# Kernel tuning notes

Hardware: AMD Instinct MI355X
Metric: run time of the kernel (lower is better)

## Reference

```python
import jax, jax.numpy as jnp
import numpy as np

HEADS = 16  # init_kwargs['heads']


def setup_inputs() -> dict:
    key = jax.random.key(0)
    k1, k2, k3, k4, k5, k6 = jax.random.split(key, 6)
    N, L, E = 2, 2048, 1024
    return {
        "values": jax.random.normal(k1, (N, L, E), dtype=jnp.float32),
        "key": jax.random.normal(k2, (N, L, E), dtype=jnp.float32),
        "query": jax.random.normal(k3, (N, L, E), dtype=jnp.float32),
        "mask": jax.random.randint(k4, (N, 1, L, L), 0, 2, dtype=jnp.int32),
        # fc_out: Linear(heads*head_dim=E, E) with bias
        "W_out": jax.random.normal(k5, (E, E), dtype=jnp.float32) / np.sqrt(E),
        "b_out": jax.random.normal(k6, (E,), dtype=jnp.float32) * 0.01,
    }


def reference(values, key, query, mask, W_out, b_out):
    N, Lq, E = query.shape
    Lk = key.shape[1]
    H = HEADS
    D = E // H  # head_dim = 64
    q = query.reshape(N, Lq, H, D)
    k = key.reshape(N, Lk, H, D)
    v = values.reshape(N, Lk, H, D)
    # energy: (N, H, Q, K)
    energy = jnp.einsum("nqhd,nkhd->nhqk", q, k)
    # masked_fill BEFORE scaling, as in the original
    energy = jnp.where(mask == 0, jnp.float32(-1e20), energy)
    attn = jax.nn.softmax(energy / np.float32(np.sqrt(D)), axis=3)
    out = jnp.einsum("nhqk,nkhd->nqhd", attn, v).reshape(N, Lq, H * D)
    return out @ W_out.T + b_out
```

## Files before the change

### kernel.cpp

```cpp
#include <hip/hip_runtime.h>

#define L_SEQ  2048
#define EMB    1024
#define NHEAD  16
#define HDIM   64
#define NBATCH 2

typedef unsigned short u16;
typedef unsigned int   u32;
typedef unsigned long long u64;
typedef short bf16x8 __attribute__((ext_vector_type(8)));
typedef float f32x4  __attribute__((ext_vector_type(4)));
typedef int   i32x4  __attribute__((ext_vector_type(4)));

static __device__ __forceinline__ u16 f2bf(float x) {
    union { float f; unsigned u; } a; a.f = x;
    unsigned r = a.u + 0x7FFFu + ((a.u >> 16) & 1u);
    return (u16)(r >> 16);
}
static __device__ __forceinline__ void cvt8(const float4& a, const float4& b, u16* o, float s) {
    o[0]=f2bf(a.x*s); o[1]=f2bf(a.y*s); o[2]=f2bf(a.z*s); o[3]=f2bf(a.w*s);
    o[4]=f2bf(b.x*s); o[5]=f2bf(b.y*s); o[6]=f2bf(b.z*s); o[7]=f2bf(b.w*s);
}

static __device__ __forceinline__ u32 cvt_pk_bf16(float lo, float hi) {
    u32 r;
    asm("v_cvt_pk_bf16_f32 %0, %1, %2" : "=v"(r) : "v"(lo), "v"(hi));
    return r;
}
static __device__ __forceinline__ void permswap32(u32 &x, u32 &y) {
    asm("v_permlane32_swap_b32 %0, %1" : "+v"(x), "+v"(y));
}
static __device__ __forceinline__ void permswap16(u32 &x, u32 &y) {
    asm("v_permlane16_swap_b32 %0, %1" : "+v"(x), "+v"(y));
}

__global__ void pack_mask(const int* __restrict__ Mg, u64* __restrict__ maskp)
{
    const int wave = threadIdx.x >> 6;
    const int lane = threadIdx.x & 63;
    const int row  = blockIdx.x * 4 + wave;
    const int* mp = Mg + (size_t)row * L_SEQ + lane;
    u64* op = maskp + (size_t)row * (L_SEQ / 64);
    for (int t = 0; t < L_SEQ / 64; ++t) {
        u64 b = __ballot(mp[t * 64] != 0);
        if (lane == 0) op[t] = b;
    }
}

__global__ __launch_bounds__(256)
void prep_qkv(const float* __restrict__ Qg, const float* __restrict__ Kg,
              const float* __restrict__ Vg, u16* __restrict__ Qb,
              u16* __restrict__ Kb, u16* __restrict__ Vt)
{
    const int t = blockIdx.x, h = blockIdx.y, n = blockIdx.z;
    const int tid = threadIdx.x;
    const int row = tid >> 2;
    const int dc  = (tid & 3) * 16;

    __shared__ u16 Vl2[64][72];

    const size_t gin = ((size_t)(n * L_SEQ) + t * 64 + row) * EMB + h * HDIM + dc;

    {
        const float qs = 0.125f * 1.44269504f;
        u16 o[16];
        cvt8(*(const float4*)(Qg + gin),     *(const float4*)(Qg + gin + 4),  o,     qs);
        cvt8(*(const float4*)(Qg + gin + 8), *(const float4*)(Qg + gin + 12), o + 8, qs);
        *(uint4*)(Qb + gin)     = *(const uint4*)o;
        *(uint4*)(Qb + gin + 8) = *(const uint4*)&o[8];
    }
    {
        u16 o[16];
        cvt8(*(const float4*)(Kg + gin),     *(const float4*)(Kg + gin + 4),  o,     1.f);
        cvt8(*(const float4*)(Kg + gin + 8), *(const float4*)(Kg + gin + 12), o + 8, 1.f);
        size_t ko = ((size_t)(n * NHEAD + h) * L_SEQ + t * 64 + row) * HDIM + dc;
        *(uint4*)(Kb + ko)     = *(const uint4*)o;
        *(uint4*)(Kb + ko + 8) = *(const uint4*)&o[8];
    }
    {
        u16 o[16];
        cvt8(*(const float4*)(Vg + gin),     *(const float4*)(Vg + gin + 4),  o,     1.f);
        cvt8(*(const float4*)(Vg + gin + 8), *(const float4*)(Vg + gin + 12), o + 8, 1.f);
        #pragma unroll
        for (int j = 0; j < 16; ++j) Vl2[dc + j][row] = o[j];
    }
    __syncthreads();
    {
        const int d  = tid >> 2;
        const int kc = (tid & 3) * 16;
        size_t vo = ((size_t)(n * NHEAD + h) * HDIM + d) * L_SEQ + t * 64 + kc;
        *(uint4*)(Vt + vo)     = *(const uint4*)&Vl2[d][kc];
        *(uint4*)(Vt + vo + 8) = *(const uint4*)&Vl2[d][kc + 8];
    }
}

__global__ void wcvt(const float* __restrict__ W, u16* __restrict__ Wb)
{
    int i = (blockIdx.x * 256 + threadIdx.x) * 8;
    float4 a = *(const float4*)(W + i);
    float4 b = *(const float4*)(W + i + 4);
    u16 o[8];
    cvt8(a, b, o, 1.f);
    *(uint4*)(Wb + i) = *(const uint4*)o;
}

__global__ __launch_bounds__(256, 4)
void attn_kernel(const u16* __restrict__ Qb, const u16* __restrict__ Kb,
                 const u16* __restrict__ Vt, const u64* __restrict__ maskp,
                 u16* __restrict__ Og)
{
    const int qblk = blockIdx.x;
    const int h    = blockIdx.y;
    const int n    = blockIdx.z;
    const int tid  = threadIdx.x;
    const int wave = tid >> 6;
    const int lane = tid & 63;
    const int l16  = lane & 15;
    const int quad = lane >> 4;

    __shared__ u16 Kl[64][72];
    __shared__ u16 Vl[64][72];

    const int q0 = qblk * 64 + wave * 16;

    bf16x8 qf[2];
    {
        const u16* qp = Qb + ((size_t)(n * L_SEQ) + q0 + l16) * EMB + h * HDIM;
        qf[0] = *(const bf16x8*)(qp + quad * 8);
        qf[1] = *(const bf16x8*)(qp + 32 + quad * 8);
    }

    f32x4 acc[4];
    #pragma unroll
    for (int c = 0; c < 4; ++c)
        #pragma unroll
        for (int r = 0; r < 4; ++r) acc[c][r] = 0.f;
    float lsum = 0.f;

    const u16* kbase = Kb + (size_t)(n * NHEAD + h) * L_SEQ * HDIM;
    const u16* vbase = Vt + (size_t)(n * NHEAD + h) * HDIM * L_SEQ;
    const u64* mbase = maskp + ((size_t)(n * L_SEQ) + q0 + l16) * (L_SEQ / 64);

    const int srow = tid >> 2;
    const int scol = (tid & 3) * 16;

    uint4 kr0, kr1, vr0, vr1;
    u64 mr;

    {
        const u16* kp = kbase + (size_t)srow * HDIM + scol;
        const u16* vp = vbase + (size_t)srow * L_SEQ + scol;
        kr0 = *(const uint4*)kp;  kr1 = *(const uint4*)(kp + 8);
        vr0 = *(const uint4*)vp;  vr1 = *(const uint4*)(vp + 8);
        mr  = mbase[0];
    }

    for (int t = 0; t < L_SEQ / 64; ++t) {
        __syncthreads();
        *(uint4*)&Kl[srow][scol]     = kr0;
        *(uint4*)&Kl[srow][scol + 8] = kr1;
        *(uint4*)&Vl[srow][scol]     = vr0;
        *(uint4*)&Vl[srow][scol + 8] = vr1;
        u64 mcur = mr;

        if (t + 1 < L_SEQ / 64) {
            const u16* kp = kbase + (size_t)((t + 1) * 64 + srow) * HDIM + scol;
            const u16* vp = vbase + (size_t)srow * L_SEQ + (t + 1) * 64 + scol;
            kr0 = *(const uint4*)kp;  kr1 = *(const uint4*)(kp + 8);
            vr0 = *(const uint4*)vp;  vr1 = *(const uint4*)(vp + 8);
            mr  = mbase[t + 1];
        }
        __syncthreads();

        f32x4 St[4];
        #pragma unroll
        for (int cc = 0; cc < 4; ++cc) {
            bf16x8 k0 = *(const bf16x8*)&Kl[cc * 16 + l16][quad * 8];
            bf16x8 k1 = *(const bf16x8*)&Kl[cc * 16 + l16][32 + quad * 8];
            f32x4 z; z[0]=0.f; z[1]=0.f; z[2]=0.f; z[3]=0.f;
            z = __builtin_amdgcn_mfma_f32_16x16x32_bf16(k0, qf[0], z, 0, 0, 0);
            z = __builtin_amdgcn_mfma_f32_16x16x32_bf16(k1, qf[1], z, 0, 0, 0);
            St[cc] = z;
        }

        u32 lo  = (u32)(mcur >> (quad * 4));
        u32 hiw = (u32)(mcur >> (quad * 4 + 32));
        u32 Dw[8];
        #pragma unroll
        for (int cc = 0; cc < 4; ++cc) {
            u32 w = (cc < 2) ? lo : hiw;
            float pv[4];
            #pragma unroll
            for (int r = 0; r < 4; ++r) {
                const int pos = (cc & 1) * 16 + r;
                int sm = (int)(w << (31 - pos)) >> 31;
                float p = __builtin_amdgcn_exp2f(St[cc][r]);
                p = __int_as_float(__float_as_int(p) & sm);
                lsum += p;
                pv[r] = p;
            }
            Dw[2 * cc]     = cvt_pk_bf16(pv[0], pv[1]);
            Dw[2 * cc + 1] = cvt_pk_bf16(pv[2], pv[3]);
        }

        #pragma unroll
        for (int kc = 0; kc < 2; ++kc) {
            u32 b0 = Dw[4 * kc + 0], b2 = Dw[4 * kc + 2];
            permswap32(b0, b2); permswap16(b0, b2);
            u32 b1 = Dw[4 * kc + 1], b3 = Dw[4 * kc + 3];
            permswap32(b1, b3); permswap16(b1, b3);
            union { i32x4 i; bf16x8 v; } pu;
            pu.i[0] = (int)b0; pu.i[1] = (int)b1; pu.i[2] = (int)b2; pu.i[3] = (int)b3;
            bf16x8 pf = pu.v;
            #pragma unroll
            for (int dc = 0; dc < 4; ++dc) {
                bf16x8 vf = *(const bf16x8*)&Vl[dc * 16 + l16][kc * 32 + quad * 8];
                acc[dc] = __builtin_amdgcn_mfma_f32_16x16x32_bf16(vf, pf, acc[dc], 0, 0, 0);
            }
        }
    }

    float s = lsum;
    s += __shfl_xor(s, 16);
    s += __shfl_xor(s, 32);
    float inv = 1.f / s;

    u16* op = Og + ((size_t)(n * L_SEQ) + q0 + l16) * EMB + h * HDIM + quad * 4;
    #pragma unroll
    for (int dc = 0; dc < 4; ++dc) {
        u32 u0 = cvt_pk_bf16(acc[dc][0] * inv, acc[dc][1] * inv);
        u32 u1 = cvt_pk_bf16(acc[dc][2] * inv, acc[dc][3] * inv);
        uint2 st; st.x = u0; st.y = u1;
        *(uint2*)(op + dc * 16) = st;
    }
}

__global__ __launch_bounds__(256, 4)
void out_gemm(const u16* __restrict__ A, const u16* __restrict__ B,
              const float* __restrict__ bias, float* __restrict__ out)
{
    const int bn  = blockIdx.x;
    const int bm  = blockIdx.y;
    const int tid = threadIdx.x;
    const int wave = tid >> 6;
    const int lane = tid & 63;
    const int l16  = lane & 15;
    const int quad = lane >> 4;
    const int wr = wave >> 1, wc = wave & 1;

    __shared__ u16 Al[64][72];
    __shared__ u16 Bl[64][72];

    f32x4 acc[2][2];
    #pragma unroll
    for (int i = 0; i < 2; ++i)
        #pragma unroll
        for (int j = 0; j < 2; ++j)
            #pragma unroll
            for (int r = 0; r < 4; ++r) acc[i][j][r] = 0.f;

    const int srow = tid >> 2;
    const int kc   = (tid & 3) * 16;

    const u16* ap = A + (size_t)(bm * 64 + srow) * EMB + kc;
    const u16* bp = B + (size_t)(bn * 64 + srow) * EMB + kc;

    uint4 ar0 = *(const uint4*)ap,        ar1 = *(const uint4*)(ap + 8);
    uint4 br0 = *(const uint4*)bp,        br1 = *(const uint4*)(bp + 8);

    for (int k0 = 0; k0 < EMB; k0 += 64) {
        __syncthreads();
        *(uint4*)&Al[srow][kc]     = ar0;
        *(uint4*)&Al[srow][kc + 8] = ar1;
        *(uint4*)&Bl[srow][kc]     = br0;
        *(uint4*)&Bl[srow][kc + 8] = br1;
        if (k0 + 64 < EMB) {
            ar0 = *(const uint4*)(ap + k0 + 64);  ar1 = *(const uint4*)(ap + k0 + 72);
            br0 = *(const uint4*)(bp + k0 + 64);  br1 = *(const uint4*)(bp + k0 + 72);
        }
        __syncthreads();

        #pragma unroll
        for (int kk = 0; kk < 2; ++kk) {
            bf16x8 af[2], bfr[2];
            #pragma unroll
            for (int i = 0; i < 2; ++i)
                af[i] = *(const bf16x8*)&Al[wr * 32 + i * 16 + l16][kk * 32 + quad * 8];
            #pragma unroll
            for (int j = 0; j < 2; ++j)
                bfr[j] = *(const bf16x8*)&Bl[wc * 32 + j * 16 + l16][kk * 32 + quad * 8];
            #pragma unroll
            for (int i = 0; i < 2; ++i)
                #pragma unroll
                for (int j = 0; j < 2; ++j)
                    acc[i][j] = __builtin_amdgcn_mfma_f32_16x16x32_bf16(af[i], bfr[j], acc[i][j], 0, 0, 0);
        }
    }

    #pragma unroll
    for (int j = 0; j < 2; ++j) {
        int col = bn * 64 + wc * 32 + j * 16 + l16;
        float bv = bias[col];
        #pragma unroll
        for (int i = 0; i < 2; ++i) {
            int row0 = bm * 64 + wr * 32 + i * 16 + quad * 4;
            #pragma unroll
            for (int r = 0; r < 4; ++r)
                out[(size_t)(row0 + r) * EMB + col] = acc[i][j][r] + bv;
        }
    }
}

extern "C" void kernel_launch(void* const* d_in, const int* in_sizes, int n_in,
                              void* d_out, int out_size, void* d_ws, size_t ws_size,
                              hipStream_t stream)
{
    const float* Vg = (const float*)d_in[0];
    const float* Kg = (const float*)d_in[1];
    const float* Qg = (const float*)d_in[2];
    const int*   Mg = (const int*)d_in[3];
    const float* Wg = (const float*)d_in[4];
    const float* Bg = (const float*)d_in[5];
    float* Og = (float*)d_out;

    const size_t QKV = (size_t)NBATCH * L_SEQ * EMB;
    char* ws = (char*)d_ws;
    u16* attn_ws = (u16*)ws;
    u16* Wb      = (u16*)(ws + QKV * 2);
    u16* Qb      = (u16*)(ws + QKV * 2 + 2 * 1024 * 1024);
    u16* Kb      = Qb + QKV;
    u16* Vt      = Kb + QKV;
    u64* maskp   = (u64*)(Vt + QKV);

    pack_mask<<<dim3(NBATCH * L_SEQ / 4), 256, 0, stream>>>(Mg, maskp);
    prep_qkv<<<dim3(L_SEQ / 64, NHEAD, NBATCH), 256, 0, stream>>>(Qg, Kg, Vg, Qb, Kb, Vt);
    wcvt<<<dim3(EMB * EMB / (256 * 8)), 256, 0, stream>>>(Wg, Wb);

    dim3 g1(L_SEQ / 64, NHEAD, NBATCH);
    attn_kernel<<<g1, 256, 0, stream>>>(Qb, Kb, Vt, maskp, attn_ws);

    dim3 g2(EMB / 64, (NBATCH * L_SEQ) / 64);
    out_gemm<<<g2, 256, 0, stream>>>(attn_ws, Wb, Bg, Og);
}
```

Before: 220.5 us.

## Process two query sub-tiles per wave to reuse K/V tiles across 128 queries

Each attention block now handles 128 queries instead of 64, and each wave computes two 16-row query sub-tiles against the same K and V fragments read from shared memory. This halves the global K/V loads and LDS traffic per query and doubles the MFMA work per LDS read. In exchange, register use per thread grows (two accumulator sets), so the launch bound drops to 2 blocks per CU, and the grid halves to 512 blocks, which reduces parallelism and the ability to hide latency.

```diff
diff --git a/kernel.cpp b/kernel.cpp
--- a/kernel.cpp
+++ b/kernel.cpp
@@ -105,7 +105,7 @@
     *(uint4*)(Wb + i) = *(const uint4*)o;
 }
 
-__global__ __launch_bounds__(256, 4)
+__global__ __launch_bounds__(256, 2)
 void attn_kernel(const u16* __restrict__ Qb, const u16* __restrict__ Kb,
                  const u16* __restrict__ Vt, const u64* __restrict__ maskp,
                  u16* __restrict__ Og)
@@ -122,38 +122,43 @@
     __shared__ u16 Kl[64][72];
     __shared__ u16 Vl[64][72];
 
-    const int q0 = qblk * 64 + wave * 16;
-
-    bf16x8 qf[2];
-    {
-        const u16* qp = Qb + ((size_t)(n * L_SEQ) + q0 + l16) * EMB + h * HDIM;
-        qf[0] = *(const bf16x8*)(qp + quad * 8);
-        qf[1] = *(const bf16x8*)(qp + 32 + quad * 8);
-    }
-
-    f32x4 acc[4];
-    #pragma unroll
-    for (int c = 0; c < 4; ++c)
-        #pragma unroll
-        for (int r = 0; r < 4; ++r) acc[c][r] = 0.f;
-    float lsum = 0.f;
+    const int q0 = qblk * 128 + wave * 32;
+
+    bf16x8 qf[2][2];
+    #pragma unroll
+    for (int qs = 0; qs < 2; ++qs) {
+        const u16* qp = Qb + ((size_t)(n * L_SEQ) + q0 + qs * 16 + l16) * EMB + h * HDIM;
+        qf[qs][0] = *(const bf16x8*)(qp + quad * 8);
+        qf[qs][1] = *(const bf16x8*)(qp + 32 + quad * 8);
+    }
+
+    f32x4 acc[2][4];
+    #pragma unroll
+    for (int qs = 0; qs < 2; ++qs)
+        #pragma unroll
+        for (int c = 0; c < 4; ++c)
+            #pragma unroll
+            for (int r = 0; r < 4; ++r) acc[qs][c][r] = 0.f;
+    float lsum[2] = {0.f, 0.f};
 
     const u16* kbase = Kb + (size_t)(n * NHEAD + h) * L_SEQ * HDIM;
     const u16* vbase = Vt + (size_t)(n * NHEAD + h) * HDIM * L_SEQ;
     const u64* mbase = maskp + ((size_t)(n * L_SEQ) + q0 + l16) * (L_SEQ / 64);
+    const int  mqs   = 16 * (L_SEQ / 64);
 
     const int srow = tid >> 2;
     const int scol = (tid & 3) * 16;
 
     uint4 kr0, kr1, vr0, vr1;
-    u64 mr;
+    u64 mr[2];
 
     {
         const u16* kp = kbase + (size_t)srow * HDIM + scol;
         const u16* vp = vbase + (size_t)srow * L_SEQ + scol;
         kr0 = *(const uint4*)kp;  kr1 = *(const uint4*)(kp + 8);
         vr0 = *(const uint4*)vp;  vr1 = *(const uint4*)(vp + 8);
-        mr  = mbase[0];
+        mr[0] = mbase[0];
+        mr[1] = mbase[mqs];
     }
 
     for (int t = 0; t < L_SEQ / 64; ++t) {
@@ -162,77 +167,91 @@
         *(uint4*)&Kl[srow][scol + 8] = kr1;
         *(uint4*)&Vl[srow][scol]     = vr0;
         *(uint4*)&Vl[srow][scol + 8] = vr1;
-        u64 mcur = mr;
+        u64 mcur0 = mr[0], mcur1 = mr[1];
 
         if (t + 1 < L_SEQ / 64) {
             const u16* kp = kbase + (size_t)((t + 1) * 64 + srow) * HDIM + scol;
             const u16* vp = vbase + (size_t)srow * L_SEQ + (t + 1) * 64 + scol;
             kr0 = *(const uint4*)kp;  kr1 = *(const uint4*)(kp + 8);
             vr0 = *(const uint4*)vp;  vr1 = *(const uint4*)(vp + 8);
-            mr  = mbase[t + 1];
+            mr[0] = mbase[t + 1];
+            mr[1] = mbase[mqs + t + 1];
         }
         __syncthreads();
 
-        f32x4 St[4];
+        const int sh = quad * 4;
+        u32 mlo[2], mhi[2];
+        mlo[0] = (u32)mcur0 >> sh;  mhi[0] = (u32)(mcur0 >> 32) >> sh;
+        mlo[1] = (u32)mcur1 >> sh;  mhi[1] = (u32)(mcur1 >> 32) >> sh;
+
+        u32 Dw[2][8];
         #pragma unroll
         for (int cc = 0; cc < 4; ++cc) {
             bf16x8 k0 = *(const bf16x8*)&Kl[cc * 16 + l16][quad * 8];
             bf16x8 k1 = *(const bf16x8*)&Kl[cc * 16 + l16][32 + quad * 8];
-            f32x4 z; z[0]=0.f; z[1]=0.f; z[2]=0.f; z[3]=0.f;
-            z = __builtin_amdgcn_mfma_f32_16x16x32_bf16(k0, qf[0], z, 0, 0, 0);
-            z = __builtin_amdgcn_mfma_f32_16x16x32_bf16(k1, qf[1], z, 0, 0, 0);
-            St[cc] = z;
-        }
-
-        u32 lo  = (u32)(mcur >> (quad * 4));
-        u32 hiw = (u32)(mcur >> (quad * 4 + 32));
-        u32 Dw[8];
-        #pragma unroll
-        for (int cc = 0; cc < 4; ++cc) {
-            u32 w = (cc < 2) ? lo : hiw;
-            float pv[4];
-            #pragma unroll
-            for (int r = 0; r < 4; ++r) {
-                const int pos = (cc & 1) * 16 + r;
-                int sm = (int)(w << (31 - pos)) >> 31;
-                float p = __builtin_amdgcn_exp2f(St[cc][r]);
-                p = __int_as_float(__float_as_int(p) & sm);
-                lsum += p;
-                pv[r] = p;
+            f32x4 z0; z0[0]=0.f; z0[1]=0.f; z0[2]=0.f; z0[3]=0.f;
+            f32x4 z1 = z0;
+            z0 = __builtin_amdgcn_mfma_f32_16x16x32_bf16(k0, qf[0][0], z0, 0, 0, 0);
+            z0 = __builtin_amdgcn_mfma_f32_16x16x32_bf16(k1, qf[0][1], z0, 0, 0, 0);
+            z1 = __builtin_amdgcn_mfma_f32_16x16x32_bf16(k0, qf[1][0], z1, 0, 0, 0);
+            z1 = __builtin_amdgcn_mfma_f32_16x16x32_bf16(k1, qf[1][1], z1, 0, 0, 0);
+
+            #pragma unroll
+            for (int qs = 0; qs < 2; ++qs) {
+                const f32x4& z = (qs == 0) ? z0 : z1;
+                u32 w = (cc < 2) ? mlo[qs] : mhi[qs];
+                float pv[4];
+                #pragma unroll
+                for (int r = 0; r < 4; ++r) {
+                    const int pos = (cc & 1) * 16 + r;
+                    int sm = (int)(w << (31 - pos)) >> 31;
+                    float p = __builtin_amdgcn_exp2f(z[r]);
+                    p = __int_as_float(__float_as_int(p) & sm);
+                    lsum[qs] += p;
+                    pv[r] = p;
+                }
+                Dw[qs][2 * cc]     = cvt_pk_bf16(pv[0], pv[1]);
+                Dw[qs][2 * cc + 1] = cvt_pk_bf16(pv[2], pv[3]);
             }
-            Dw[2 * cc]     = cvt_pk_bf16(pv[0], pv[1]);
-            Dw[2 * cc + 1] = cvt_pk_bf16(pv[2], pv[3]);
         }
 
         #pragma unroll
         for (int kc = 0; kc < 2; ++kc) {
-            u32 b0 = Dw[4 * kc + 0], b2 = Dw[4 * kc + 2];
-            permswap32(b0, b2); permswap16(b0, b2);
-            u32 b1 = Dw[4 * kc + 1], b3 = Dw[4 * kc + 3];
-            permswap32(b1, b3); permswap16(b1, b3);
-            union { i32x4 i; bf16x8 v; } pu;
-            pu.i[0] = (int)b0; pu.i[1] = (int)b1; pu.i[2] = (int)b2; pu.i[3] = (int)b3;
-            bf16x8 pf = pu.v;
+            bf16x8 pf[2];
+            #pragma unroll
+            for (int qs = 0; qs < 2; ++qs) {
+                u32 b0 = Dw[qs][4 * kc + 0], b2 = Dw[qs][4 * kc + 2];
+                permswap32(b0, b2); permswap16(b0, b2);
+                u32 b1 = Dw[qs][4 * kc + 1], b3 = Dw[qs][4 * kc + 3];
+                permswap32(b1, b3); permswap16(b1, b3);
+                union { i32x4 i; bf16x8 v; } pu;
+                pu.i[0] = (int)b0; pu.i[1] = (int)b1; pu.i[2] = (int)b2; pu.i[3] = (int)b3;
+                pf[qs] = pu.v;
+            }
             #pragma unroll
             for (int dc = 0; dc < 4; ++dc) {
                 bf16x8 vf = *(const bf16x8*)&Vl[dc * 16 + l16][kc * 32 + quad * 8];
-                acc[dc] = __builtin_amdgcn_mfma_f32_16x16x32_bf16(vf, pf, acc[dc], 0, 0, 0);
+                acc[0][dc] = __builtin_amdgcn_mfma_f32_16x16x32_bf16(vf, pf[0], acc[0][dc], 0, 0, 0);
+                acc[1][dc] = __builtin_amdgcn_mfma_f32_16x16x32_bf16(vf, pf[1], acc[1][dc], 0, 0, 0);
             }
         }
     }
 
-    float s = lsum;
-    s += __shfl_xor(s, 16);
-    s += __shfl_xor(s, 32);
-    float inv = 1.f / s;
-
-    u16* op = Og + ((size_t)(n * L_SEQ) + q0 + l16) * EMB + h * HDIM + quad * 4;
-    #pragma unroll
-    for (int dc = 0; dc < 4; ++dc) {
-        u32 u0 = cvt_pk_bf16(acc[dc][0] * inv, acc[dc][1] * inv);
-        u32 u1 = cvt_pk_bf16(acc[dc][2] * inv, acc[dc][3] * inv);
-        uint2 st; st.x = u0; st.y = u1;
-        *(uint2*)(op + dc * 16) = st;
+    #pragma unroll
+    for (int qs = 0; qs < 2; ++qs) {
+        float s = lsum[qs];
+        s += __shfl_xor(s, 16);
+        s += __shfl_xor(s, 32);
+        float inv = 1.f / s;
+
+        u16* op = Og + ((size_t)(n * L_SEQ) + q0 + qs * 16 + l16) * EMB + h * HDIM + quad * 4;
+        #pragma unroll
+        for (int dc = 0; dc < 4; ++dc) {
+            u32 u0 = cvt_pk_bf16(acc[qs][dc][0] * inv, acc[qs][dc][1] * inv);
+            u32 u1 = cvt_pk_bf16(acc[qs][dc][2] * inv, acc[qs][dc][3] * inv);
+            uint2 st; st.x = u0; st.y = u1;
+            *(uint2*)(op + dc * 16) = st;
+        }
     }
 }
 
@@ -337,7 +356,7 @@
     prep_qkv<<<dim3(L_SEQ / 64, NHEAD, NBATCH), 256, 0, stream>>>(Qg, Kg, Vg, Qb, Kb, Vt);
     wcvt<<<dim3(EMB * EMB / (256 * 8)), 256, 0, stream>>>(Wg, Wb);
 
-    dim3 g1(L_SEQ / 64, NHEAD, NBATCH);
+    dim3 g1(L_SEQ / 128, NHEAD, NBATCH);
     attn_kernel<<<g1, 256, 0, stream>>>(Qb, Kb, Vt, maskp, attn_ws);
 
     dim3 g2(EMB / 64, (NBATCH * L_SEQ) / 64);
```

Result: no change. 220.4 us (-0.0%).
